# Kernel optimization log

Measured on AMD Instinct MI355X. Metric: run time of the kernel, lower is better.

Reference implementation:

```python
import jax, jax.numpy as jnp
import numpy as np

N = 50000
E = 1_600_000
H = 128          # hidden_dim
HEADS = 4
PH = H // 2      # platform embedding dim = 64
LRELU_SLOPE = 0.2
BN_EPS = 1e-5


def _lin_init(key, fan_in, fan_out):
    return jax.random.normal(key, (fan_in, fan_out), jnp.float32) / np.sqrt(fan_in)


def setup_inputs() -> dict:
    key = jax.random.key(0)
    ks = jax.random.split(key, 32)
    inp = {}
    inp["x"] = jax.random.normal(ks[0], (N, 10), jnp.float32)
    inp["edge_index"] = jax.random.randint(ks[1], (2, E), 0, N, jnp.int32)
    inp["platform_x"] = jax.random.normal(ks[2], (1, 4), jnp.float32)
    # node encoder
    inp["node_W"] = _lin_init(ks[3], 10, H); inp["node_b"] = jnp.zeros((H,))
    # platform encoder
    inp["plat_W"] = _lin_init(ks[4], 4, PH); inp["plat_b"] = jnp.zeros((PH,))
    # GAT layers: W [in, heads*out], att vectors [1, heads, out], bias [heads*out]
    inp["g1_W"] = _lin_init(ks[5], H, H)
    inp["g1_asrc"] = jax.random.normal(ks[6], (1, HEADS, H // HEADS)) * 0.1
    inp["g1_adst"] = jax.random.normal(ks[7], (1, HEADS, H // HEADS)) * 0.1
    inp["g1_b"] = jnp.zeros((H,))
    inp["g2_W"] = _lin_init(ks[8], H, H)
    inp["g2_asrc"] = jax.random.normal(ks[9], (1, HEADS, H // HEADS)) * 0.1
    inp["g2_adst"] = jax.random.normal(ks[10], (1, HEADS, H // HEADS)) * 0.1
    inp["g2_b"] = jnp.zeros((H,))
    inp["g3_W"] = _lin_init(ks[11], H, H)
    inp["g3_asrc"] = jax.random.normal(ks[12], (1, 1, H)) * 0.1
    inp["g3_adst"] = jax.random.normal(ks[13], (1, 1, H)) * 0.1
    inp["g3_b"] = jnp.zeros((H,))
    # BatchNorm (eval mode: running_mean=0, running_var=1)
    for i, k in zip((1, 2, 3), (ks[14], ks[15], ks[16])):
        inp[f"bn{i}_g"] = jnp.ones((H,)) + 0.1 * jax.random.normal(k, (H,))
        inp[f"bn{i}_b"] = jnp.zeros((H,))
    # classifier: 192 -> 128 -> 64 -> 3
    inp["c1_W"] = _lin_init(ks[17], H + PH, H); inp["c1_b"] = jnp.zeros((H,))
    inp["c2_W"] = _lin_init(ks[18], H, PH);     inp["c2_b"] = jnp.zeros((PH,))
    inp["c3_W"] = _lin_init(ks[19], PH, 3);     inp["c3_b"] = jnp.zeros((3,))
    return inp


def gat_conv(x, src, dst, W, a_src, a_dst, b, heads, out_dim, n):
    # PyG GATConv (eval, self-loops already appended): gather -> edge score ->
    # segment softmax over destination -> scatter-add.
    h = (x @ W).reshape(n, heads, out_dim)              # [N, heads, out]
    al_s = jnp.sum(h * a_src, axis=-1)                  # [N, heads]
    al_d = jnp.sum(h * a_dst, axis=-1)                  # [N, heads]
    e = jax.nn.leaky_relu(al_s[src] + al_d[dst], LRELU_SLOPE)  # [E, heads]
    m = jax.ops.segment_max(e, dst, num_segments=n)
    m = jnp.where(jnp.isfinite(m), m, 0.0)
    ex = jnp.exp(e - m[dst])
    s = jax.ops.segment_sum(ex, dst, num_segments=n)
    alpha = ex / (s[dst] + 1e-16)                       # [E, heads]
    out = jax.ops.segment_sum(alpha[:, :, None] * h[src], dst, num_segments=n)
    return out.reshape(n, heads * out_dim) + b


def bn_eval(x, g, b):
    # running_mean=0, running_var=1 -> x / sqrt(1+eps) * g + b
    return x * (g / np.sqrt(1.0 + BN_EPS)) + b


def reference(x, edge_index, platform_x, node_W, node_b, plat_W, plat_b,
              g1_W, g1_asrc, g1_adst, g1_b, g2_W, g2_asrc, g2_adst, g2_b,
              g3_W, g3_asrc, g3_adst, g3_b, bn1_g, bn1_b, bn2_g, bn2_b,
              bn3_g, bn3_b, c1_W, c1_b, c2_W, c2_b, c3_W, c3_b):
    n = x.shape[0]
    loops = jnp.arange(n, dtype=edge_index.dtype)
    src = jnp.concatenate([edge_index[0], loops])
    dst = jnp.concatenate([edge_index[1], loops])

    h = jax.nn.relu(x @ node_W + node_b)
    h = gat_conv(h, src, dst, g1_W, g1_asrc, g1_adst, g1_b, HEADS, H // HEADS, n)
    h = jax.nn.relu(bn_eval(h, bn1_g, bn1_b))
    h = gat_conv(h, src, dst, g2_W, g2_asrc, g2_adst, g2_b, HEADS, H // HEADS, n)
    h = jax.nn.relu(bn_eval(h, bn2_g, bn2_b))
    h = gat_conv(h, src, dst, g3_W, g3_asrc, g3_adst, g3_b, 1, H, n)
    h = jax.nn.relu(bn_eval(h, bn3_g, bn3_b))

    p = jax.nn.relu(platform_x @ plat_W + plat_b)       # [1, PH]
    p = jnp.broadcast_to(p[0:1], (n, PH))
    h = jnp.concatenate([h, p], axis=1)                 # [N, H+PH]

    h = jax.nn.relu(h @ c1_W + c1_b)
    h = jax.nn.relu(h @ c2_W + c2_b)
    return h @ c3_W + c3_b                              # [N, 3]
```

## Files before the change

kernel.cpp:

```cpp
#include <hip/hip_runtime.h>
#include <hip/hip_bf16.h>
#include <hip/hip_fp16.h>

#define LRELU 0.2f
#define BN_INVS 0.99999500003749968f

__global__ __launch_bounds__(256) void k_initdeg(int* deg, int n) {
    int i = blockIdx.x * 256 + threadIdx.x;
    if (i < n) deg[i] = 1;
}

__global__ __launch_bounds__(256) void k_count(const int* __restrict__ ei, int* deg, int E) {
    int e = blockIdx.x * 256 + threadIdx.x;
    if (e < E) atomicAdd(&deg[__builtin_nontemporal_load(&ei[E + e]) ? (ei[E + e]) : ei[E + e]], 1);
}

__global__ __launch_bounds__(1024) void k_scan1(const int* __restrict__ deg, int* row_ptr,
                                                int* bsum, int n) {
    __shared__ int sm[1024];
    int t = threadIdx.x, g = blockIdx.x * 1024 + t;
    sm[t] = (g < n) ? deg[g] : 0;
    __syncthreads();
    for (int off = 1; off < 1024; off <<= 1) {
        int x = (t >= off) ? sm[t - off] : 0;
        __syncthreads();
        sm[t] += x;
        __syncthreads();
    }
    if (g < n) row_ptr[g + 1] = sm[t];
    if (t == 1023) bsum[blockIdx.x] = sm[t];
}

__global__ void k_scan2(const int* bsum, int* boff, int nb) {
    if (threadIdx.x == 0 && blockIdx.x == 0) {
        int s = 0;
        for (int i = 0; i < nb; ++i) { boff[i] = s; s += bsum[i]; }
    }
}

__global__ __launch_bounds__(1024) void k_scan3(int* row_ptr, const int* boff, int n) {
    int g = blockIdx.x * 1024 + threadIdx.x;
    if (g < n) row_ptr[g + 1] += boff[blockIdx.x];
    if (g == 0) row_ptr[0] = 0;
}

__global__ __launch_bounds__(256) void k_cursor(const int* __restrict__ rp, int* cur, int n) {
    int i = blockIdx.x * 256 + threadIdx.x;
    if (i < n) cur[i] = rp[i];
}

__global__ __launch_bounds__(256) void k_scatter(const int* __restrict__ ei, int* cur, int* col,
                                                 int E, int n) {
    int g = blockIdx.x & 7;
    int W = (n + 7) >> 3;
    int lo = g * W;
    int hi = min(n, lo + W);
    int nb = gridDim.x >> 3;
    int bi = blockIdx.x >> 3;
    int stride = nb * 256;
    for (int t = bi * 256 + threadIdx.x; t < E; t += stride) {
        int d = __builtin_nontemporal_load(ei + E + t);
        if (d >= lo && d < hi) {
            int s = __builtin_nontemporal_load(ei + t);
            int p = atomicAdd(&cur[d], 1);
            col[p] = s;
        }
    }
    for (int v = lo + bi * 256 + threadIdx.x; v < hi; v += stride) {
        int p = atomicAdd(&cur[v], 1);
        col[p] = v;
    }
}

__global__ __launch_bounds__(256) void k_node_enc(const float* __restrict__ x,
                                                  const float* __restrict__ W,
                                                  const float* __restrict__ b,
                                                  float* __restrict__ h, int n) {
    __shared__ float Ws[1280];
    __shared__ float bs[128];
    for (int i = threadIdx.x; i < 1280; i += 256) Ws[i] = W[i];
    if (threadIdx.x < 128) bs[threadIdx.x] = b[threadIdx.x];
    __syncthreads();
    int idx = blockIdx.x * 256 + threadIdx.x;
    if (idx >= n * 32) return;
    int v = idx >> 5, q = idx & 31;
    float xr[10];
#pragma unroll
    for (int i = 0; i < 10; ++i) xr[i] = x[v * 10 + i];
    float o[4];
#pragma unroll
    for (int j = 0; j < 4; ++j) {
        int c = q * 4 + j;
        float s = bs[c];
#pragma unroll
        for (int i = 0; i < 10; ++i) s += xr[i] * Ws[i * 128 + c];
        o[j] = fmaxf(s, 0.f);
    }
    *(float4*)(h + (size_t)v * 128 + q * 4) = make_float4(o[0], o[1], o[2], o[3]);
}

template <int M, bool ADD_BIAS, bool RELU, bool HALF_OUT = false>
__global__ __launch_bounds__(256) void k_gemm64(const float* __restrict__ A,
                                                const float* __restrict__ B,
                                                const float* __restrict__ bias,
                                                float* __restrict__ C, int n) {
    __shared__ float AsT[32][68];
    __shared__ float Bs[32][68];
    int tid = threadIdx.x;
    int row0 = blockIdx.x * 64;
    int col0 = blockIdx.y * 64;
    int ct = tid & 15, rt = tid >> 4;
    float4 acc[4];
#pragma unroll
    for (int i = 0; i < 4; ++i) acc[i] = make_float4(0.f, 0.f, 0.f, 0.f);

    for (int kc = 0; kc < 128; kc += 32) {
#pragma unroll
        for (int i = 0; i < 2; ++i) {
            int f = tid + i * 256;
            int r = f >> 3;
            int kq = (f & 7) * 4;
            float4 v = make_float4(0.f, 0.f, 0.f, 0.f);
            int gr = row0 + r;
            if (gr < n) v = *(const float4*)(A + (size_t)gr * 128 + kc + kq);
            AsT[kq + 0][r] = v.x;
            AsT[kq + 1][r] = v.y;
            AsT[kq + 2][r] = v.z;
            AsT[kq + 3][r] = v.w;
        }
#pragma unroll
        for (int i = 0; i < 2; ++i) {
            int f = tid + i * 256;
            int r = f >> 4;
            int c4 = (f & 15) * 4;
            *(float4*)(&Bs[r][c4]) = *(const float4*)(B + (size_t)(kc + r) * M + col0 + c4);
        }
        __syncthreads();
#pragma unroll
        for (int k = 0; k < 32; ++k) {
            float4 av = *(const float4*)(&AsT[k][rt * 4]);
            float4 bv = *(const float4*)(&Bs[k][ct * 4]);
            acc[0].x += av.x * bv.x; acc[0].y += av.x * bv.y; acc[0].z += av.x * bv.z; acc[0].w += av.x * bv.w;
            acc[1].x += av.y * bv.x; acc[1].y += av.y * bv.y; acc[1].z += av.y * bv.z; acc[1].w += av.y * bv.w;
            acc[2].x += av.z * bv.x; acc[2].y += av.z * bv.y; acc[2].z += av.z * bv.z; acc[2].w += av.z * bv.w;
            acc[3].x += av.w * bv.x; acc[3].y += av.w * bv.y; acc[3].z += av.w * bv.z; acc[3].w += av.w * bv.w;
        }
        __syncthreads();
    }
    float4 bb = make_float4(0.f, 0.f, 0.f, 0.f);
    if (ADD_BIAS) bb = *(const float4*)(bias + col0 + ct * 4);
#pragma unroll
    for (int i = 0; i < 4; ++i) {
        int gr = row0 + rt * 4 + i;
        if (gr < n) {
            float4 v = acc[i];
            if (ADD_BIAS) {
                v.x += bb.x; v.y += bb.y; v.z += bb.z; v.w += bb.w;
            }
            if (RELU) {
                v.x = fmaxf(v.x, 0.f); v.y = fmaxf(v.y, 0.f);
                v.z = fmaxf(v.z, 0.f); v.w = fmaxf(v.w, 0.f);
            }
            if (HALF_OUT) {
                __half hb[4];
                hb[0] = __float2half(v.x);
                hb[1] = __float2half(v.y);
                hb[2] = __float2half(v.z);
                hb[3] = __float2half(v.w);
                __half* C16 = reinterpret_cast<__half*>(C);
                *(ushort4*)(C16 + (size_t)gr * M + col0 + ct * 4) = *(ushort4*)hb;
            } else {
                *(float4*)(C + (size_t)gr * M + col0 + ct * 4) = v;
            }
        }
    }
}

template <int HEADS>
__global__ __launch_bounds__(256) void k_al(const __half* __restrict__ hw,
                                            const float* __restrict__ asrc,
                                            const float* __restrict__ adst,
                                            float* __restrict__ al_s, float* __restrict__ al_d,
                                            int n) {
    int wid = (blockIdx.x * 256 + threadIdx.x) >> 6;
    int l = threadIdx.x & 63;
    if (wid >= n) return;
    unsigned raw = *(const unsigned*)(hw + (size_t)wid * 128 + 2 * l);
    __half2 hp = *reinterpret_cast<__half2*>(&raw);
    float2 hv = __half22float2(hp);
    int c0 = 2 * l;
    if (HEADS == 4) {
        int h = l >> 4, dd = c0 & 31;
        float s = hv.x * asrc[h * 32 + dd] + hv.y * asrc[h * 32 + dd + 1];
        float d = hv.x * adst[h * 32 + dd] + hv.y * adst[h * 32 + dd + 1];
#pragma unroll
        for (int off = 1; off < 16; off <<= 1) {
            s += __shfl_xor(s, off);
            d += __shfl_xor(d, off);
        }
        if ((l & 15) == 0) {
            al_s[wid * 4 + h] = s;
            al_d[wid * 4 + h] = d;
        }
    } else {
        float s = hv.x * asrc[c0] + hv.y * asrc[c0 + 1];
        float d = hv.x * adst[c0] + hv.y * adst[c0 + 1];
#pragma unroll
        for (int off = 1; off < 64; off <<= 1) {
            s += __shfl_xor(s, off);
            d += __shfl_xor(d, off);
        }
        if (l == 0) {
            al_s[wid] = s;
            al_d[wid] = d;
        }
    }
}

template <int HEADS>
__global__ __launch_bounds__(256) void k_softagg(const int* __restrict__ rp,
                                                 const int* __restrict__ col,
                                                 const float* __restrict__ al_s,
                                                 const float* __restrict__ al_d,
                                                 const __half* __restrict__ hw,
                                                 const float* __restrict__ gb,
                                                 const float* __restrict__ bng,
                                                 const float* __restrict__ bnb,
                                                 float* __restrict__ hout, int n) {
    constexpr int CAP = 128;
    __shared__ int ss[4][CAP];
    __shared__ __align__(16) float se[4][CAP * HEADS];
    int v = (blockIdx.x * 256 + threadIdx.x) >> 6;
    int l = threadIdx.x & 63;
    int w = threadIdx.x >> 6;
    if (v >= n) return;
    int start = rp[v], end = rp[v + 1];
    int deg = end - start;

    float ad[HEADS], m[HEADS], s[HEADS], inv[HEADS];
#pragma unroll
    for (int h = 0; h < HEADS; ++h) {
        ad[h] = al_d[v * HEADS + h];
        m[h] = -1e30f;
        s[h] = 0.f;
    }

    if (deg <= CAP) {
        for (int p = start + l; p < end; p += 64) {
            int src = col[p];
            float eh[HEADS];
            if (HEADS == 4) {
                float4 t4 = *(const float4*)(al_s + (size_t)src * 4);
                eh[0] = t4.x; eh[1] = t4.y; eh[2] = t4.z; eh[3] = t4.w;
            } else {
                eh[0] = al_s[src];
            }
#pragma unroll
            for (int h = 0; h < HEADS; ++h) {
                float e = eh[h] + ad[h];
                eh[h] = (e >= 0.f) ? e : LRELU * e;
                m[h] = fmaxf(m[h], eh[h]);
            }
            int idx = p - start;
            ss[w][idx] = src;
            if (HEADS == 4)
                *(float4*)(&se[w][idx * 4]) = make_float4(eh[0], eh[1], eh[2], eh[3]);
            else
                se[w][idx] = eh[0];
        }
#pragma unroll
        for (int off = 1; off < 64; off <<= 1)
#pragma unroll
            for (int h = 0; h < HEADS; ++h) m[h] = fmaxf(m[h], __shfl_xor(m[h], off));

        for (int idx = l; idx < deg; idx += 64) {
            if (HEADS == 4) {
                float4 e4 = *(float4*)(&se[w][idx * 4]);
                e4.x = __expf(e4.x - m[0]);
                e4.y = __expf(e4.y - m[1]);
                e4.z = __expf(e4.z - m[2]);
                e4.w = __expf(e4.w - m[3]);
                *(float4*)(&se[w][idx * 4]) = e4;
                s[0] += e4.x; s[1] += e4.y; s[2] += e4.z; s[3] += e4.w;
            } else {
                float a = __expf(se[w][idx] - m[0]);
                se[w][idx] = a;
                s[0] += a;
            }
        }
#pragma unroll
        for (int off = 1; off < 64; off <<= 1)
#pragma unroll
            for (int h = 0; h < HEADS; ++h) s[h] += __shfl_xor(s[h], off);
#pragma unroll
        for (int h = 0; h < HEADS; ++h) inv[h] = 1.f / (s[h] + 1e-16f);

        int qe = l >> 4;
        int li = l & 15;
        int c8 = li * 8;
        int hd = (HEADS == 4) ? (li >> 2) : 0;
        float invh = inv[hd];
        float acc[8] = {0.f, 0.f, 0.f, 0.f, 0.f, 0.f, 0.f, 0.f};
        for (int p = start + qe; p < end; p += 4) {
            int idx = p - start;
            int s0 = ss[w][idx];
            float a0 = (HEADS == 4) ? se[w][idx * 4 + hd] : se[w][idx];
            uint4 r = *(const uint4*)(hw + (size_t)s0 * 128 + c8);
            float2 f0 = __half22float2(*reinterpret_cast<__half2*>(&r.x));
            float2 f1 = __half22float2(*reinterpret_cast<__half2*>(&r.y));
            float2 f2 = __half22float2(*reinterpret_cast<__half2*>(&r.z));
            float2 f3 = __half22float2(*reinterpret_cast<__half2*>(&r.w));
            acc[0] += a0 * f0.x; acc[1] += a0 * f0.y;
            acc[2] += a0 * f1.x; acc[3] += a0 * f1.y;
            acc[4] += a0 * f2.x; acc[5] += a0 * f2.y;
            acc[6] += a0 * f3.x; acc[7] += a0 * f3.y;
        }
#pragma unroll
        for (int j = 0; j < 8; ++j) {
            acc[j] += __shfl_xor(acc[j], 16);
            acc[j] += __shfl_xor(acc[j], 32);
        }
        if (l < 16) {
#pragma unroll
            for (int half = 0; half < 2; ++half) {
                int c4 = c8 + half * 4;
                float4 g4 = *(const float4*)(gb + c4);
                float4 bg = *(const float4*)(bng + c4);
                float4 bbv = *(const float4*)(bnb + c4);
                float4 o;
                o.x = fmaxf((acc[half * 4 + 0] * invh + g4.x) * (bg.x * BN_INVS) + bbv.x, 0.f);
                o.y = fmaxf((acc[half * 4 + 1] * invh + g4.y) * (bg.y * BN_INVS) + bbv.y, 0.f);
                o.z = fmaxf((acc[half * 4 + 2] * invh + g4.z) * (bg.z * BN_INVS) + bbv.z, 0.f);
                o.w = fmaxf((acc[half * 4 + 3] * invh + g4.w) * (bg.w * BN_INVS) + bbv.w, 0.f);
                *(float4*)(hout + (size_t)v * 128 + c4) = o;
            }
        }
        return;
    }

    for (int p = start + l; p < end; p += 64) {
        int src = col[p];
        float eh[HEADS];
        if (HEADS == 4) {
            float4 t4 = *(const float4*)(al_s + (size_t)src * 4);
            eh[0] = t4.x; eh[1] = t4.y; eh[2] = t4.z; eh[3] = t4.w;
        } else {
            eh[0] = al_s[src];
        }
#pragma unroll
        for (int h = 0; h < HEADS; ++h) {
            float e = eh[h] + ad[h];
            e = (e >= 0.f) ? e : LRELU * e;
            float nm = fmaxf(m[h], e);
            s[h] = s[h] * __expf(m[h] - nm) + __expf(e - nm);
            m[h] = nm;
        }
    }
#pragma unroll
    for (int off = 1; off < 64; off <<= 1) {
#pragma unroll
        for (int h = 0; h < HEADS; ++h) {
            float om = __shfl_xor(m[h], off), os = __shfl_xor(s[h], off);
            float nm = fmaxf(m[h], om);
            s[h] = s[h] * __expf(m[h] - nm) + os * __expf(om - nm);
            m[h] = nm;
        }
    }
#pragma unroll
    for (int h = 0; h < HEADS; ++h) inv[h] = 1.f / (s[h] + 1e-16f);

    int ew = l >> 5;
    int li = l & 31;
    int c4 = 4 * li;
    int hd = (HEADS == 4) ? (li >> 3) : 0;
    float mh = m[hd], invh = inv[hd], adh = ad[hd];
    float4 acc = make_float4(0.f, 0.f, 0.f, 0.f);
    for (int p = start + ew; p < end; p += 2) {
        int s0 = col[p];
        float t = al_s[(size_t)s0 * HEADS + hd] + adh;
        float e0 = (t >= 0.f) ? t : LRELU * t;
        float a0 = __expf(e0 - mh);
        uint2 r0 = *(const uint2*)(hw + (size_t)s0 * 128 + c4);
        float2 f00 = __half22float2(*reinterpret_cast<__half2*>(&r0.x));
        float2 f01 = __half22float2(*reinterpret_cast<__half2*>(&r0.y));
        acc.x += a0 * f00.x;
        acc.y += a0 * f00.y;
        acc.z += a0 * f01.x;
        acc.w += a0 * f01.y;
    }
    acc.x += __shfl_xor(acc.x, 32);
    acc.y += __shfl_xor(acc.y, 32);
    acc.z += __shfl_xor(acc.z, 32);
    acc.w += __shfl_xor(acc.w, 32);
    if (l < 32) {
        float4 g4 = *(const float4*)(gb + c4);
        float4 bg = *(const float4*)(bng + c4);
        float4 bbv = *(const float4*)(bnb + c4);
        float4 o;
        o.x = fmaxf((acc.x * invh + g4.x) * (bg.x * BN_INVS) + bbv.x, 0.f);
        o.y = fmaxf((acc.y * invh + g4.y) * (bg.y * BN_INVS) + bbv.y, 0.f);
        o.z = fmaxf((acc.z * invh + g4.z) * (bg.z * BN_INVS) + bbv.z, 0.f);
        o.w = fmaxf((acc.w * invh + g4.w) * (bg.w * BN_INVS) + bbv.w, 0.f);
        *(float4*)(hout + (size_t)v * 128 + c4) = o;
    }
}

__global__ void k_pconst(const float* __restrict__ px, const float* __restrict__ pW,
                         const float* __restrict__ pb, const float* __restrict__ c1W,
                         const float* __restrict__ c1b, float* __restrict__ cvec) {
    __shared__ float p[64];
    int t = threadIdx.x;
    if (t < 64) {
        float s = pb[t];
#pragma unroll
        for (int i = 0; i < 4; ++i) s += px[i] * pW[i * 64 + t];
        p[t] = fmaxf(s, 0.f);
    }
    __syncthreads();
    if (t < 128) {
        float s = c1b[t];
#pragma unroll
        for (int j = 0; j < 64; ++j) s += p[j] * c1W[(128 + j) * 128 + t];
        cvec[t] = s;
    }
}

__global__ __launch_bounds__(256) void k_c3(const float* __restrict__ h5,
                                            const float* __restrict__ W,
                                            const float* __restrict__ b, float* __restrict__ out,
                                            int n) {
    __shared__ float Ws[192];
    __shared__ float bs[3];
    if (threadIdx.x < 192) Ws[threadIdx.x] = W[threadIdx.x];
    if (threadIdx.x < 3) bs[threadIdx.x] = b[threadIdx.x];
    __syncthreads();
    int v = blockIdx.x * 256 + threadIdx.x;
    if (v >= n) return;
    float a0 = bs[0], a1 = bs[1], a2 = bs[2];
#pragma unroll
    for (int k4 = 0; k4 < 16; ++k4) {
        float4 xv = *(const float4*)(h5 + (size_t)v * 64 + k4 * 4);
        int k = k4 * 4;
        a0 += xv.x * Ws[k * 3 + 0] + xv.y * Ws[k * 3 + 3] + xv.z * Ws[k * 3 + 6] + xv.w * Ws[k * 3 + 9];
        a1 += xv.x * Ws[k * 3 + 1] + xv.y * Ws[k * 3 + 4] + xv.z * Ws[k * 3 + 7] + xv.w * Ws[k * 3 + 10];
        a2 += xv.x * Ws[k * 3 + 2] + xv.y * Ws[k * 3 + 5] + xv.z * Ws[k * 3 + 8] + xv.w * Ws[k * 3 + 11];
    }
    out[v * 3 + 0] = a0;
    out[v * 3 + 1] = a1;
    out[v * 3 + 2] = a2;
}

extern "C" void kernel_launch(void* const* d_in, const int* in_sizes, int n_in,
                              void* d_out, int out_size, void* d_ws, size_t ws_size,
                              hipStream_t stream) {
    const float* x      = (const float*)d_in[0];
    const int*   ei     = (const int*)d_in[1];
    const float* px     = (const float*)d_in[2];
    const float* node_W = (const float*)d_in[3];
    const float* node_b = (const float*)d_in[4];
    const float* plat_W = (const float*)d_in[5];
    const float* plat_b = (const float*)d_in[6];
    const float* g1_W = (const float*)d_in[7];
    const float* g1_as = (const float*)d_in[8];
    const float* g1_ad = (const float*)d_in[9];
    const float* g1_b = (const float*)d_in[10];
    const float* g2_W = (const float*)d_in[11];
    const float* g2_as = (const float*)d_in[12];
    const float* g2_ad = (const float*)d_in[13];
    const float* g2_b = (const float*)d_in[14];
    const float* g3_W = (const float*)d_in[15];
    const float* g3_as = (const float*)d_in[16];
    const float* g3_ad = (const float*)d_in[17];
    const float* g3_b = (const float*)d_in[18];
    const float* bn1_g = (const float*)d_in[19];
    const float* bn1_b = (const float*)d_in[20];
    const float* bn2_g = (const float*)d_in[21];
    const float* bn2_b = (const float*)d_in[22];
    const float* bn3_g = (const float*)d_in[23];
    const float* bn3_b = (const float*)d_in[24];
    const float* c1_W = (const float*)d_in[25];
    const float* c1_b = (const float*)d_in[26];
    const float* c2_W = (const float*)d_in[27];
    const float* c2_b = (const float*)d_in[28];
    const float* c3_W = (const float*)d_in[29];
    const float* c3_b = (const float*)d_in[30];

    const int N = in_sizes[0] / 10;
    const int E = in_sizes[1] / 2;
    const int ET = E + N;

    char* w = (char*)d_ws;
    auto alloc = [&](size_t bytes) {
        void* p = (void*)w;
        w += (bytes + 255) & ~(size_t)255;
        return p;
    };
    int*   col     = (int*)alloc((size_t)ET * 4);
    int*   deg     = (int*)alloc((size_t)N * 4);
    int*   row_ptr = (int*)alloc((size_t)(N + 1) * 4);
    int*   bsum    = (int*)alloc(256 * 4);
    int*   boff    = (int*)alloc(256 * 4);
    float* al_s    = (float*)alloc((size_t)N * 4 * 4);
    float* al_d    = (float*)alloc((size_t)N * 4 * 4);
    float* bufA    = (float*)alloc((size_t)N * 128 * 4);
    float* bufB    = (float*)alloc((size_t)N * 128 * 4);
    float* cvec    = (float*)alloc(128 * 4);
    float* out     = (float*)d_out;
    __half* h16    = (__half*)bufB;

    const int NB = (N + 1023) / 1024;

    k_initdeg<<<(N + 255) / 256, 256, 0, stream>>>(deg, N);
    k_count<<<(E + 255) / 256, 256, 0, stream>>>(ei, deg, E);
    k_scan1<<<NB, 1024, 0, stream>>>(deg, row_ptr, bsum, N);
    k_scan2<<<1, 64, 0, stream>>>(bsum, boff, NB);
    k_scan3<<<NB, 1024, 0, stream>>>(row_ptr, boff, N);
    k_cursor<<<(N + 255) / 256, 256, 0, stream>>>(row_ptr, deg, N);
    k_scatter<<<3328, 256, 0, stream>>>(ei, deg, col, E, N);

    k_node_enc<<<(N * 32 + 255) / 256, 256, 0, stream>>>(x, node_W, node_b, bufA, N);

    const dim3 g128((N + 63) / 64, 2);
    const dim3 g64((N + 63) / 64, 1);
    const int gWave = (N * 64 + 255) / 256;

    k_gemm64<128, false, false, true><<<g128, 256, 0, stream>>>(bufA, g1_W, nullptr, (float*)h16, N);
    k_al<4><<<gWave, 256, 0, stream>>>(h16, g1_as, g1_ad, al_s, al_d, N);
    k_softagg<4><<<gWave, 256, 0, stream>>>(row_ptr, col, al_s, al_d, h16, g1_b, bn1_g, bn1_b, bufA, N);

    k_gemm64<128, false, false, true><<<g128, 256, 0, stream>>>(bufA, g2_W, nullptr, (float*)h16, N);
    k_al<4><<<gWave, 256, 0, stream>>>(h16, g2_as, g2_ad, al_s, al_d, N);
    k_softagg<4><<<gWave, 256, 0, stream>>>(row_ptr, col, al_s, al_d, h16, g2_b, bn2_g, bn2_b, bufA, N);

    k_gemm64<128, false, false, true><<<g128, 256, 0, stream>>>(bufA, g3_W, nullptr, (float*)h16, N);
    k_al<1><<<gWave, 256, 0, stream>>>(h16, g3_as, g3_ad, al_s, al_d, N);
    k_softagg<1><<<gWave, 256, 0, stream>>>(row_ptr, col, al_s, al_d, h16, g3_b, bn3_g, bn3_b, bufA, N);

    k_pconst<<<1, 128, 0, stream>>>(px, plat_W, plat_b, c1_W, c1_b, cvec);

    k_gemm64<128, true, true><<<g128, 256, 0, stream>>>(bufA, c1_W, cvec, bufB, N);
    k_gemm64<64, true, true><<<g64, 256, 0, stream>>>(bufB, c2_W, c2_b, bufA, N);
    k_c3<<<(N + 255) / 256, 256, 0, stream>>>(bufA, c3_W, c3_b, out, N);
}
```

Measured before the change: 628.7 us.

## Bucket edges by destination range before CSR scatter to avoid repeated edge scans

Replaces the CSR scatter, in which each of 8 destination-range groups rescanned the whole destination array, with a two-pass scheme. The first pass reads the edges once, uses per-block shared histograms and a global atomic cursor per bucket, and writes packed (dst,src) pairs into 8 contiguous buckets held in a reused workspace buffer. The second pass scatters each bucket's pairs into the column array with per-node atomics, as before. This removes roughly 8x redundant reads of the edge list, at the cost of an extra 8-byte-per-edge write and read plus one more kernel launch. It also tidies the degree-count kernel's odd double load.

```diff
diff --git a/kernel.cpp b/kernel.cpp
--- a/kernel.cpp
+++ b/kernel.cpp
@@ -12,7 +12,10 @@
 
 __global__ __launch_bounds__(256) void k_count(const int* __restrict__ ei, int* deg, int E) {
     int e = blockIdx.x * 256 + threadIdx.x;
-    if (e < E) atomicAdd(&deg[__builtin_nontemporal_load(&ei[E + e]) ? (ei[E + e]) : ei[E + e]], 1);
+    if (e < E) {
+        int d = __builtin_nontemporal_load(ei + E + e);
+        atomicAdd(&deg[d], 1);
+    }
 }
 
 __global__ __launch_bounds__(1024) void k_scan1(const int* __restrict__ deg, int* row_ptr,
@@ -44,29 +47,64 @@
     if (g == 0) row_ptr[0] = 0;
 }
 
-__global__ __launch_bounds__(256) void k_cursor(const int* __restrict__ rp, int* cur, int n) {
+__global__ __launch_bounds__(256) void k_cursor(const int* __restrict__ rp, int* cur, int* bcur,
+                                                int n) {
     int i = blockIdx.x * 256 + threadIdx.x;
     if (i < n) cur[i] = rp[i];
-}
-
-__global__ __launch_bounds__(256) void k_scatter(const int* __restrict__ ei, int* cur, int* col,
-                                                 int E, int n) {
-    int g = blockIdx.x & 7;
+    if (i < 8) {
+        int W = (n + 7) >> 3;
+        bcur[i] = rp[min(n, i * W)];
+    }
+}
+
+__global__ __launch_bounds__(256) void k_bucket(const int* __restrict__ ei, int E, int n,
+                                                unsigned long long* __restrict__ pairs,
+                                                int* __restrict__ bcur) {
+    __shared__ int hist[8], base[8];
     int W = (n + 7) >> 3;
-    int lo = g * W;
-    int hi = min(n, lo + W);
-    int nb = gridDim.x >> 3;
-    int bi = blockIdx.x >> 3;
+    int chunk = (E + gridDim.x - 1) / gridDim.x;
+    int lo = blockIdx.x * chunk;
+    int hi = min(E, lo + chunk);
+    if (threadIdx.x < 8) hist[threadIdx.x] = 0;
+    __syncthreads();
+    for (int t = lo + threadIdx.x; t < hi; t += 256) {
+        int d = ei[E + t];
+        atomicAdd(&hist[d / W], 1);
+    }
+    __syncthreads();
+    if (threadIdx.x < 8) {
+        base[threadIdx.x] = atomicAdd(&bcur[threadIdx.x], hist[threadIdx.x]);
+        hist[threadIdx.x] = 0;
+    }
+    __syncthreads();
+    for (int t = lo + threadIdx.x; t < hi; t += 256) {
+        int d = ei[E + t];
+        int s = ei[t];
+        int b = d / W;
+        int pos = base[b] + atomicAdd(&hist[b], 1);
+        pairs[pos] = ((unsigned long long)(unsigned)d << 32) | (unsigned)s;
+    }
+}
+
+__global__ __launch_bounds__(256) void k_scatter2(const unsigned long long* __restrict__ pairs,
+                                                  const int* __restrict__ rp,
+                                                  const int* __restrict__ bcur,
+                                                  int* cur, int* col, int n) {
+    int b = blockIdx.x & 7;
+    int W = (n + 7) >> 3;
+    int lo = rp[min(n, b * W)];
+    int hi = bcur[b];
+    int nb = gridDim.x >> 3, bi = blockIdx.x >> 3;
     int stride = nb * 256;
-    for (int t = bi * 256 + threadIdx.x; t < E; t += stride) {
-        int d = __builtin_nontemporal_load(ei + E + t);
-        if (d >= lo && d < hi) {
-            int s = __builtin_nontemporal_load(ei + t);
-            int p = atomicAdd(&cur[d], 1);
-            col[p] = s;
-        }
-    }
-    for (int v = lo + bi * 256 + threadIdx.x; v < hi; v += stride) {
+    for (int t = lo + bi * 256 + threadIdx.x; t < hi; t += stride) {
+        unsigned long long pr = pairs[t];
+        int d = (int)(pr >> 32);
+        int s = (int)(pr & 0xffffffffu);
+        int p = atomicAdd(&cur[d], 1);
+        col[p] = s;
+    }
+    int vlo = b * W, vhi = min(n, vlo + W);
+    for (int v = vlo + bi * 256 + threadIdx.x; v < vhi; v += stride) {
         int p = atomicAdd(&cur[v], 1);
         col[p] = v;
     }
@@ -500,6 +538,7 @@
     int*   row_ptr = (int*)alloc((size_t)(N + 1) * 4);
     int*   bsum    = (int*)alloc(256 * 4);
     int*   boff    = (int*)alloc(256 * 4);
+    int*   bcur    = (int*)alloc(8 * 4);
     float* al_s    = (float*)alloc((size_t)N * 4 * 4);
     float* al_d    = (float*)alloc((size_t)N * 4 * 4);
     float* bufA    = (float*)alloc((size_t)N * 128 * 4);
@@ -507,6 +546,7 @@
     float* cvec    = (float*)alloc(128 * 4);
     float* out     = (float*)d_out;
     __half* h16    = (__half*)bufB;
+    unsigned long long* pairs = (unsigned long long*)bufA;
 
     const int NB = (N + 1023) / 1024;
 
@@ -515,8 +555,9 @@
     k_scan1<<<NB, 1024, 0, stream>>>(deg, row_ptr, bsum, N);
     k_scan2<<<1, 64, 0, stream>>>(bsum, boff, NB);
     k_scan3<<<NB, 1024, 0, stream>>>(row_ptr, boff, N);
-    k_cursor<<<(N + 255) / 256, 256, 0, stream>>>(row_ptr, deg, N);
-    k_scatter<<<3328, 256, 0, stream>>>(ei, deg, col, E, N);
+    k_cursor<<<(N + 255) / 256, 256, 0, stream>>>(row_ptr, deg, bcur, N);
+    k_bucket<<<1024, 256, 0, stream>>>(ei, E, N, pairs, bcur);
+    k_scatter2<<<3328, 256, 0, stream>>>(pairs, row_ptr, bcur, deg, col, N);
 
     k_node_enc<<<(N * 32 + 255) / 256, 256, 0, stream>>>(x, node_W, node_b, bufA, N);
 
```

After: 645.7 us. 2.7% more time.
